# Performance work log

Measured on AMD Instinct MI355X. Metric: run time of the kernel, lower is better.

## Reference

```python
import jax, jax.numpy as jnp
import numpy as np

EPS = 1e-5

def _bn_eval(x, gamma, beta, rmean, rvar):
    # BatchNorm1d in eval mode: elementwise affine using running stats
    inv = jax.lax.rsqrt(rvar + EPS)
    return (x - rmean) * inv * gamma + beta

def setup_inputs() -> dict:
    key = jax.random.key(0)
    ks = jax.random.split(key, 12)
    N, F, H, C = 16384, 512, 512, 128
    x = jax.random.normal(ks[0], (N, F), dtype=jnp.float32)
    a = jax.random.uniform(ks[1], (N, N), dtype=jnp.float32)
    w1 = jax.random.normal(ks[2], (F, H), dtype=jnp.float32) * (1.0 / np.sqrt(F))
    b1 = jax.random.normal(ks[3], (H,), dtype=jnp.float32) * 0.01
    w2 = jax.random.normal(ks[4], (H, C), dtype=jnp.float32) * (1.0 / np.sqrt(H))
    b2 = jax.random.normal(ks[5], (C,), dtype=jnp.float32) * 0.01
    g1 = jax.random.normal(ks[6], (F,), dtype=jnp.float32) * 0.1 + 1.0
    beta1 = jax.random.normal(ks[7], (F,), dtype=jnp.float32) * 0.01
    rm1 = jax.random.normal(ks[8], (F,), dtype=jnp.float32) * 0.1
    rv1 = jax.random.uniform(ks[9], (F,), dtype=jnp.float32, minval=0.5, maxval=1.5)
    g2 = jax.random.normal(ks[10], (H,), dtype=jnp.float32) * 0.1 + 1.0
    beta2 = jax.random.normal(ks[11], (H,), dtype=jnp.float32) * 0.01
    rm2 = jnp.zeros((H,), dtype=jnp.float32)
    rv2 = jnp.ones((H,), dtype=jnp.float32)
    return {"x": x, "a": a, "w1": w1, "b1": b1, "w2": w2, "b2": b2,
            "g1": g1, "beta1": beta1, "rm1": rm1, "rv1": rv1,
            "g2": g2, "beta2": beta2, "rm2": rm2, "rv2": rv2}

def reference(x, a, w1, b1, w2, b2, g1, beta1, rm1, rv1, g2, beta2, rm2, rv2):
    # x: [N, F] node features, a: [N, N] adjacency
    x2 = _bn_eval(x, g1, beta1, rm1, rv1)          # norm1
    x2 = a @ x2                                     # message passing (aggregation)
    x2 = x2 @ w1 + b1                               # conv1 (Linear)
    x2 = jax.nn.relu(x2)
    x2 = _bn_eval(x2, g2, beta2, rm2, rv2)          # norm2
    # dropout is identity in eval mode
    x1 = a @ x2                                     # second aggregation
    x1 = x1 @ w2 + b2                               # conv2 (Linear)
    return (x1, x2)
```

## Files before the change

### kernel.cpp

```cpp
#include <hip/hip_runtime.h>
#include <hip/hip_bf16.h>

typedef unsigned short u16;
typedef unsigned int u32;
typedef __attribute__((ext_vector_type(4))) float f32x4;
typedef __attribute__((ext_vector_type(8))) short bf16x8;

#define DEVI static __device__ __forceinline__

DEVI u16 f2bf(float f) {
  u32 u = __builtin_bit_cast(u32, f);
  u += 0x7fffu + ((u >> 16) & 1u);
  return (u16)(u >> 16);
}

DEVI void gload_lds16(const void* g, void* l) {
  __builtin_amdgcn_global_load_lds(
      (const __attribute__((address_space(1))) u32*)g,
      (__attribute__((address_space(3))) u32*)l, 16, 0, 0);
}

template<int N> DEVI void wait_vm() {
  if constexpr (N == 0)      asm volatile("s_waitcnt vmcnt(0)" ::: "memory");
  else if constexpr (N == 5) asm volatile("s_waitcnt vmcnt(5)" ::: "memory");
  else if constexpr (N == 6) asm volatile("s_waitcnt vmcnt(6)" ::: "memory");
  else if constexpr (N == 8) asm volatile("s_waitcnt vmcnt(8)" ::: "memory");
  else                       asm volatile("s_waitcnt vmcnt(0)" ::: "memory");
}
DEVI void lgkm_barrier() {
  asm volatile("s_waitcnt lgkmcnt(0)\n\ts_barrier" ::: "memory");
}

struct Aregs { f32x4 v0, v1; uint4 h; };

template<int BN_FULL, int BN_T, bool AF32, int EPI, int NSPL, int KSPL,
         int DEPTH>
__global__ __launch_bounds__(512, 4)
void gk(const void* __restrict__ Ap, const u16* __restrict__ Bt,
        const int Kfull, const int M, float* __restrict__ outf,
        u16* __restrict__ outh,
        const float* __restrict__ e0, const float* __restrict__ e1,
        const float* __restrict__ e2, const float* __restrict__ e3,
        const float* __restrict__ e4)
{
  constexpr int BM = 64, BK = 64;
  constexpr int TN = BN_T / 8;
  constexpr int MF = 4, NF = TN / 16;
  constexpr int ABYTES = BM * BK * 2;
  constexpr int SLICE = TN * BK * 2;
  constexpr int LB = SLICE / 1024;
  constexpr int LA = AF32 ? 2 : 1;
  constexpr int NB = DEPTH + 1;
  constexpr int VMW = DEPTH * (LA + LB);
  constexpr int SPL = NSPL * KSPL;

  __shared__ char smem[2 * ABYTES + NB * 8 * SLICE];

  const int tid = threadIdx.x;
  const int w = tid >> 6, l = tid & 63;
  const int l15 = l & 15, l4 = l >> 4;

  const int G8 = gridDim.x >> 3;
  const int q = (blockIdx.x & 7) * G8 + (blockIdx.x >> 3);
  const int sub = q % SPL;
  const int m0 = (q / SPL) * BM;
  const int nh = (NSPL == 2) ? sub : 0;
  const int kc = (KSPL == 2) ? sub : 0;
  const int n0 = nh * BN_T;
  const int klen = Kfull / KSPL;
  const int k0 = kc * klen;
  const int NT = klen / BK;

  auto off = [&](int row, int chq) -> int {
    return row * 128 + ((chq ^ (row & 7)) << 4);
  };

  const int ar = tid >> 3, ac = tid & 7;
  const int apos = off(ar, ac);
  const size_t Abase = (size_t)(m0 + ar) * Kfull + k0 + (size_t)ac * 8;

  char* const bslice = smem + 2 * ABYTES + w * SLICE;

  f32x4 acc[MF][NF];
#pragma unroll
  for (int i = 0; i < MF; ++i)
#pragma unroll
    for (int j = 0; j < NF; ++j) acc[i][j] = (f32x4){0.f, 0.f, 0.f, 0.f};

  Aregs R0, R1;

  auto issueA = [&](Aregs& R, int t) {
    if constexpr (AF32) {
      const float* p = (const float*)Ap + Abase + (size_t)t * BK;
      R.v0 = *(const f32x4*)p;
      R.v1 = *(const f32x4*)(p + 4);
    } else {
      const u16* p = (const u16*)Ap + Abase + (size_t)t * BK;
      R.h = *(const uint4*)p;
    }
  };
  auto writeA = [&](int nb, Aregs& R) {
    uint4 pk;
    if constexpr (AF32) {
      pk.x = (u32)f2bf(R.v0[0]) | ((u32)f2bf(R.v0[1]) << 16);
      pk.y = (u32)f2bf(R.v0[2]) | ((u32)f2bf(R.v0[3]) << 16);
      pk.z = (u32)f2bf(R.v1[0]) | ((u32)f2bf(R.v1[1]) << 16);
      pk.w = (u32)f2bf(R.v1[2]) | ((u32)f2bf(R.v1[3]) << 16);
    } else {
      pk = R.h;
    }
    *(uint4*)(smem + nb * ABYTES + apos) = pk;
  };
  auto issueB = [&](int nb, int t) {
    const char* bsrc = (const char*)Bt +
                       ((size_t)(n0 + w * TN) * Kfull + k0 +
                        (size_t)t * BK) * 2;
    char* bd = bslice + nb * (8 * SLICE);
#pragma unroll
    for (int i = 0; i < LB; ++i) {
      const int p = i * 1024 + l * 16;
      const int nl = p >> 7;
      const int chq = ((p & 127) >> 4) ^ (nl & 7);
      gload_lds16(bsrc + (size_t)nl * ((size_t)Kfull * 2) + chq * 16,
                  bd + i * 1024);
    }
  };
  auto compute = [&](int ab, int bb) {
    const char* A = smem + ab * ABYTES;
    const char* Bs = bslice + bb * (8 * SLICE);
#pragma unroll
    for (int kk = 0; kk < 2; ++kk) {
      bf16x8 af[MF];
      uint4 bfr[NF];
#pragma unroll
      for (int mi = 0; mi < MF; ++mi)
        af[mi] = *(const bf16x8*)(A + off(mi * 16 + l15, kk * 4 + l4));
#pragma unroll
      for (int ni = 0; ni < NF; ++ni)
        bfr[ni] = *(const uint4*)(Bs + off(ni * 16 + l15, kk * 4 + l4));
      __builtin_amdgcn_s_setprio(1);
#pragma unroll
      for (int mi = 0; mi < MF; ++mi)
#pragma unroll
        for (int ni = 0; ni < NF; ++ni)
          acc[mi][ni] = __builtin_amdgcn_mfma_f32_16x16x32_bf16(
              af[mi], __builtin_bit_cast(bf16x8, bfr[ni]), acc[mi][ni],
              0, 0, 0);
      __builtin_amdgcn_s_setprio(0);
    }
  };

  issueB(0, 0);
  issueA(R0, 0);
  issueA(R1, NT > 1 ? 1 : 0);
  if constexpr (DEPTH == 2) issueB(1, NT > 1 ? 1 : 0);
  writeA(0, R0);
  lgkm_barrier();

  int bc = 0, bi = DEPTH % NB;
  int t2 = 0;

#define SUBSTEP(RI, RW, ABUF)                                                \
  {                                                                          \
    const int tA = (t2 + 2 < NT) ? t2 + 2 : NT - 1;                          \
    const int tB = (t2 + DEPTH < NT) ? t2 + DEPTH : NT - 1;                  \
    issueA(RI, tA);                                                          \
    issueB(bi, tB);                                                          \
    wait_vm<VMW>();                                                          \
    compute(ABUF, bc);                                                       \
    writeA(ABUF ^ 1, RW);                                                    \
    lgkm_barrier();                                                          \
    bc = (bc + 1 == NB) ? 0 : bc + 1;                                        \
    bi = (bi + 1 == NB) ? 0 : bi + 1;                                        \
    ++t2;                                                                    \
  }

  for (int it = 0; it < NT / 2; ++it) {
    SUBSTEP(R0, R1, 0);
    SUBSTEP(R1, R0, 1);
  }
#undef SUBSTEP

  wait_vm<0>();

  const int mrow0 = m0 + l4 * 4;
#pragma unroll
  for (int ni = 0; ni < NF; ++ni) {
    const int n = n0 + w * TN + ni * 16 + l15;
    if constexpr (EPI == 0) {
#pragma unroll
      for (int mi = 0; mi < MF; ++mi) {
        const int m = mrow0 + mi * 16;
        ushort4 o;
        o.x = f2bf(acc[mi][ni][0]);
        o.y = f2bf(acc[mi][ni][1]);
        o.z = f2bf(acc[mi][ni][2]);
        o.w = f2bf(acc[mi][ni][3]);
        *(ushort4*)(outh + (size_t)n * M + m) = o;
      }
    } else if constexpr (EPI == 1) {
      const float b1v = e0[n];
      const float sc = e1[n] * rsqrtf(e4[n] + 1e-5f);
      const float sh = e2[n] - e3[n] * sc;
#pragma unroll
      for (int mi = 0; mi < MF; ++mi)
#pragma unroll
        for (int r = 0; r < 4; ++r) {
          const float s = fmaxf(acc[mi][ni][r] + b1v, 0.f);
          outf[(size_t)(mrow0 + mi * 16 + r) * BN_FULL + n] = s * sc + sh;
        }
    } else {
      float* Pout = outf + (size_t)kc * ((size_t)M * BN_FULL);
#pragma unroll
      for (int mi = 0; mi < MF; ++mi)
#pragma unroll
        for (int r = 0; r < 4; ++r)
          Pout[(size_t)(mrow0 + mi * 16 + r) * BN_FULL + n] = acc[mi][ni][r];
    }
  }
}

__global__ __launch_bounds__(256)
void bn1_cast_k(const float* __restrict__ x, const float* __restrict__ g,
                const float* __restrict__ be, const float* __restrict__ rm,
                const float* __restrict__ rv, u16* __restrict__ out)
{
  const size_t i8 = ((size_t)blockIdx.x * 256 + threadIdx.x) * 8;
  const f32x4 v0 = *(const f32x4*)(x + i8);
  const f32x4 v1 = *(const f32x4*)(x + i8 + 4);
  const int f0 = (int)(i8 & 511);
  u16 u[8];
#pragma unroll
  for (int e = 0; e < 8; ++e) {
    const int f = f0 + e;
    const float sc = g[f] * rsqrtf(rv[f] + 1e-5f);
    const float v = (e < 4) ? v0[e] : v1[e - 4];
    u[e] = f2bf((v - rm[f]) * sc + be[f]);
  }
  uint4 o;
  o.x = (u32)u[0] | ((u32)u[1] << 16);
  o.y = (u32)u[2] | ((u32)u[3] << 16);
  o.z = (u32)u[4] | ((u32)u[5] << 16);
  o.w = (u32)u[6] | ((u32)u[7] << 16);
  *(uint4*)(out + i8) = o;
}

__global__ __launch_bounds__(256)
void tcvt_k(const float* __restrict__ in, u16* __restrict__ out, int rowlen)
{
  const int o = blockIdx.x * 256 + threadIdx.x;
  out[o] = f2bf(in[(size_t)(o & 511) * rowlen + (o >> 9)]);
}

__global__ __launch_bounds__(256)
void comb_k(const float* __restrict__ P, const float* __restrict__ b2,
            float* __restrict__ out)
{
  const size_t i4 = ((size_t)blockIdx.x * 256 + threadIdx.x) * 4;
  const f32x4 p0 = *(const f32x4*)(P + i4);
  const f32x4 p1 = *(const f32x4*)(P + (size_t)16384 * 128 + i4);
  const int f0 = (int)(i4 & 127);
  f32x4 o;
#pragma unroll
  for (int e = 0; e < 4; ++e) o[e] = p0[e] + p1[e] + b2[f0 + e];
  *(f32x4*)(out + i4) = o;
}

extern "C" void kernel_launch(void* const* d_in, const int* in_sizes, int n_in,
                              void* d_out, int out_size, void* d_ws, size_t ws_size,
                              hipStream_t stream)
{
  const float* x   = (const float*)d_in[0];
  const float* a   = (const float*)d_in[1];
  const float* w1  = (const float*)d_in[2];
  const float* b1  = (const float*)d_in[3];
  const float* w2  = (const float*)d_in[4];
  const float* b2  = (const float*)d_in[5];
  const float* g1  = (const float*)d_in[6];
  const float* be1 = (const float*)d_in[7];
  const float* rm1 = (const float*)d_in[8];
  const float* rv1 = (const float*)d_in[9];
  const float* g2  = (const float*)d_in[10];
  const float* be2 = (const float*)d_in[11];
  const float* rm2 = (const float*)d_in[12];
  const float* rv2 = (const float*)d_in[13];

  constexpr int N = 16384, F = 512, H = 512, C = 128;
  float* x1 = (float*)d_out;
  float* x2 = (float*)d_out + (size_t)N * C;

  char* wsp = (char*)d_ws;
  u16* xb  = (u16*)wsp;  wsp += (size_t)N * F * 2;
  u16* t_t = (u16*)wsp;  wsp += (size_t)H * N * 2;
  u16* z_t = (u16*)wsp;  wsp += (size_t)C * N * 2;
  u16* w1t = (u16*)wsp;  wsp += (size_t)H * F * 2;
  u16* w2t = (u16*)wsp;  wsp += (size_t)C * H * 2;
  float* Pp = (float*)wsp;

  bn1_cast_k<<<(N * F / 8) / 256, 256, 0, stream>>>(x, g1, be1, rm1, rv1, xb);
  tcvt_k<<<(F * H) / 256, 256, 0, stream>>>(w1, w1t, H);
  tcvt_k<<<(H * C) / 256, 256, 0, stream>>>(w2, w2t, C);

  gk<512, 256, false, 0, 2, 1, 1><<<512, 512, 0, stream>>>(
      xb, w1t, F, N, nullptr, t_t, nullptr, nullptr, nullptr, nullptr, nullptr);

  gk<512, 256, true, 1, 2, 1, 1><<<512, 512, 0, stream>>>(
      a, t_t, N, N, x2, nullptr, b1, g2, be2, rm2, rv2);

  gk<128, 128, true, 0, 1, 1, 2><<<256, 512, 0, stream>>>(
      x2, w2t, H, N, nullptr, z_t, nullptr, nullptr, nullptr, nullptr, nullptr);

  gk<128, 128, true, 2, 1, 2, 2><<<512, 512, 0, stream>>>(
      a, z_t, N, N, Pp, nullptr, nullptr, nullptr, nullptr, nullptr, nullptr);

  comb_k<<<(N * C / 4) / 256, 256, 0, stream>>>(Pp, b2, x1);
}
```

Baseline: 700.5 us.

## Retile big aggregation GEMM with BM=128/BK=32, split-K and XCD-aware block mapping

```diff
diff --git a/kernel.cpp b/kernel.cpp
--- a/kernel.cpp
+++ b/kernel.cpp
@@ -33,26 +33,25 @@
 
 struct Aregs { f32x4 v0, v1; uint4 h; };
 
-template<int BN_FULL, int BN_T, bool AF32, int EPI, int NSPL, int KSPL,
-         int DEPTH>
+template<int BM, int BN_FULL, int BN_T, int BK, bool AF32, int EPI, int XMAP,
+         int NSPL, int KSPL, int DEPTH>
 __global__ __launch_bounds__(512, 4)
 void gk(const void* __restrict__ Ap, const u16* __restrict__ Bt,
         const int Kfull, const int M, float* __restrict__ outf,
-        u16* __restrict__ outh,
-        const float* __restrict__ e0, const float* __restrict__ e1,
-        const float* __restrict__ e2, const float* __restrict__ e3,
-        const float* __restrict__ e4)
-{
-  constexpr int BM = 64, BK = 64;
+        u16* __restrict__ outh)
+{
   constexpr int TN = BN_T / 8;
-  constexpr int MF = 4, NF = TN / 16;
+  constexpr int MF = BM / 16, NF = TN / 16, KK = BK / 32;
   constexpr int ABYTES = BM * BK * 2;
   constexpr int SLICE = TN * BK * 2;
   constexpr int LB = SLICE / 1024;
   constexpr int LA = AF32 ? 2 : 1;
   constexpr int NB = DEPTH + 1;
   constexpr int VMW = DEPTH * (LA + LB);
+  constexpr int CPR = BK / 8;
   constexpr int SPL = NSPL * KSPL;
+  static_assert(BM * BK == 4096, "one 16B A chunk per thread");
+  static_assert(DEPTH <= 2, "DEPTH=3 wait algebra unsound (see r9 post-mortem)");
 
   __shared__ char smem[2 * ABYTES + NB * 8 * SLICE];
 
@@ -60,22 +59,32 @@
   const int w = tid >> 6, l = tid & 63;
   const int l15 = l & 15, l4 = l >> 4;
 
-  const int G8 = gridDim.x >> 3;
-  const int q = (blockIdx.x & 7) * G8 + (blockIdx.x >> 3);
-  const int sub = q % SPL;
-  const int m0 = (q / SPL) * BM;
-  const int nh = (NSPL == 2) ? sub : 0;
-  const int kc = (KSPL == 2) ? sub : 0;
+  int m0, nh, kc;
+  if constexpr (XMAP == 1) {
+    const int xcd = blockIdx.x & 7;
+    const int combo = xcd >> 1;
+    nh = combo & 1;
+    kc = combo >> 1;
+    m0 = ((int)(blockIdx.x >> 3) + (xcd & 1) * 64) * BM;
+  } else {
+    const int G8 = gridDim.x >> 3;
+    const int q = (blockIdx.x & 7) * G8 + (blockIdx.x >> 3);
+    const int sub = q % SPL;
+    m0 = (q / SPL) * BM;
+    nh = (NSPL == 2) ? sub : 0;
+    kc = (KSPL == 2) ? sub : 0;
+  }
   const int n0 = nh * BN_T;
   const int klen = Kfull / KSPL;
   const int k0 = kc * klen;
   const int NT = klen / BK;
 
   auto off = [&](int row, int chq) -> int {
-    return row * 128 + ((chq ^ (row & 7)) << 4);
-  };
-
-  const int ar = tid >> 3, ac = tid & 7;
+    if constexpr (BK == 64) return row * 128 + ((chq ^ (row & 7)) << 4);
+    else                    return row * 64 + ((chq ^ ((row >> 1) & 3)) << 4);
+  };
+
+  const int ar = tid / CPR, ac = tid % CPR;
   const int apos = off(ar, ac);
   const size_t Abase = (size_t)(m0 + ar) * Kfull + k0 + (size_t)ac * 8;
 
@@ -119,8 +128,9 @@
 #pragma unroll
     for (int i = 0; i < LB; ++i) {
       const int p = i * 1024 + l * 16;
-      const int nl = p >> 7;
-      const int chq = ((p & 127) >> 4) ^ (nl & 7);
+      const int nl = (BK == 64) ? (p >> 7) : (p >> 6);
+      const int chp = (p & (BK * 2 - 1)) >> 4;
+      const int chq = (BK == 64) ? (chp ^ (nl & 7)) : (chp ^ ((nl >> 1) & 3));
       gload_lds16(bsrc + (size_t)nl * ((size_t)Kfull * 2) + chq * 16,
                   bd + i * 1024);
     }
@@ -129,7 +139,7 @@
     const char* A = smem + ab * ABYTES;
     const char* Bs = bslice + bb * (8 * SLICE);
 #pragma unroll
-    for (int kk = 0; kk < 2; ++kk) {
+    for (int kk = 0; kk < KK; ++kk) {
       bf16x8 af[MF];
       uint4 bfr[NF];
 #pragma unroll
@@ -198,17 +208,6 @@
         o.w = f2bf(acc[mi][ni][3]);
         *(ushort4*)(outh + (size_t)n * M + m) = o;
       }
-    } else if constexpr (EPI == 1) {
-      const float b1v = e0[n];
-      const float sc = e1[n] * rsqrtf(e4[n] + 1e-5f);
-      const float sh = e2[n] - e3[n] * sc;
-#pragma unroll
-      for (int mi = 0; mi < MF; ++mi)
-#pragma unroll
-        for (int r = 0; r < 4; ++r) {
-          const float s = fmaxf(acc[mi][ni][r] + b1v, 0.f);
-          outf[(size_t)(mrow0 + mi * 16 + r) * BN_FULL + n] = s * sc + sh;
-        }
     } else {
       float* Pout = outf + (size_t)kc * ((size_t)M * BN_FULL);
 #pragma unroll
@@ -250,6 +249,27 @@
 {
   const int o = blockIdx.x * 256 + threadIdx.x;
   out[o] = f2bf(in[(size_t)(o & 511) * rowlen + (o >> 9)]);
+}
+
+__global__ __launch_bounds__(256)
+void comb_bn_k(const float* __restrict__ P, const float* __restrict__ b1,
+               const float* __restrict__ g2, const float* __restrict__ be2,
+               const float* __restrict__ rm2, const float* __restrict__ rv2,
+               float* __restrict__ out)
+{
+  const size_t i4 = ((size_t)blockIdx.x * 256 + threadIdx.x) * 4;
+  const f32x4 p0 = *(const f32x4*)(P + i4);
+  const f32x4 p1 = *(const f32x4*)(P + (size_t)16384 * 512 + i4);
+  const int f0 = (int)(i4 & 511);
+  f32x4 o;
+#pragma unroll
+  for (int e = 0; e < 4; ++e) {
+    const int f = f0 + e;
+    const float s = fmaxf(p0[e] + p1[e] + b1[f], 0.f);
+    const float sc = g2[f] * rsqrtf(rv2[f] + 1e-5f);
+    o[e] = s * sc + (be2[f] - rm2[f] * sc);
+  }
+  *(f32x4*)(out + i4) = o;
 }
 
 __global__ __launch_bounds__(256)
@@ -301,17 +321,20 @@
   tcvt_k<<<(F * H) / 256, 256, 0, stream>>>(w1, w1t, H);
   tcvt_k<<<(H * C) / 256, 256, 0, stream>>>(w2, w2t, C);
 
-  gk<512, 256, false, 0, 2, 1, 1><<<512, 512, 0, stream>>>(
-      xb, w1t, F, N, nullptr, t_t, nullptr, nullptr, nullptr, nullptr, nullptr);
-
-  gk<512, 256, true, 1, 2, 1, 1><<<512, 512, 0, stream>>>(
-      a, t_t, N, N, x2, nullptr, b1, g2, be2, rm2, rv2);
-
-  gk<128, 128, true, 0, 1, 1, 2><<<256, 512, 0, stream>>>(
-      x2, w2t, H, N, nullptr, z_t, nullptr, nullptr, nullptr, nullptr, nullptr);
-
-  gk<128, 128, true, 2, 1, 2, 2><<<512, 512, 0, stream>>>(
-      a, z_t, N, N, Pp, nullptr, nullptr, nullptr, nullptr, nullptr, nullptr);
+  gk<64, 512, 256, 64, false, 0, 0, 2, 1, 1><<<512, 512, 0, stream>>>(
+      xb, w1t, F, N, nullptr, t_t);
+
+  gk<128, 512, 256, 32, true, 2, 1, 2, 2, 2><<<512, 512, 0, stream>>>(
+      a, t_t, N, N, Pp, nullptr);
+
+  comb_bn_k<<<(N * H / 4) / 256, 256, 0, stream>>>(Pp, b1, g2, be2, rm2, rv2,
+                                                   x2);
+
+  gk<64, 128, 128, 64, true, 0, 0, 1, 1, 2><<<256, 512, 0, stream>>>(
+      x2, w2t, H, N, nullptr, z_t);
+
+  gk<64, 128, 128, 64, true, 2, 0, 1, 2, 2><<<512, 512, 0, stream>>>(
+      a, z_t, N, N, Pp, nullptr);
 
   comb_k<<<(N * C / 4) / 256, 256, 0, stream>>>(Pp, b2, x1);
 }
```

Result: slower. 1.388 ms (+98.1%).
